# Kernel optimization log

Hardware: AMD Instinct MI355X
Metric: run time of the kernel (lower is better)

The kernel has to match this reference:

```python
import jax, jax.numpy as jnp
import numpy as np


def rotate_half(x):
    d = x.shape[-1] // 2
    return jnp.concatenate([-x[..., d:], x[..., :d]], axis=-1)


def setup_inputs() -> dict:
    key = jax.random.key(0)
    ks = jax.random.split(key, 8)
    B, T, C, H = 2, 2048, 2048, 16
    hd = C // H
    x = jax.random.normal(ks[0], (B, T, C), dtype=jnp.float32)
    # realistic RoPE tables
    inv_freq = 1.0 / (10000.0 ** (jnp.arange(0, hd, 2, dtype=jnp.float32) / hd))
    t = jnp.arange(T, dtype=jnp.float32)
    freqs = jnp.einsum('t,f->tf', t, inv_freq)
    emb = jnp.concatenate([freqs, freqs], axis=-1)  # [T, hd]
    cos = jnp.cos(emb)
    sin = jnp.sin(emb)
    mask = jnp.tril(jnp.ones((T, T), dtype=bool))[None, None]  # causal [1,1,T,T]
    s = C ** -0.5
    Wq = jax.random.normal(ks[1], (C, C), dtype=jnp.float32) * s
    Wk = jax.random.normal(ks[2], (C, C), dtype=jnp.float32) * s
    Wv = jax.random.normal(ks[3], (C, C), dtype=jnp.float32) * s
    Wo = jax.random.normal(ks[4], (C, C), dtype=jnp.float32) * s
    return {"x": x, "cos": cos, "sin": sin, "mask": mask,
            "Wq": Wq, "Wk": Wk, "Wv": Wv, "Wo": Wo}


def reference(x, cos, sin, mask, Wq, Wk, Wv, Wo):
    B, T, C = x.shape
    H = 16
    hd = C // H
    scale = hd ** -0.5
    # projections: torch Linear stores W as [out,in], y = x @ W^T
    def proj(W):
        return jnp.einsum('btc,dc->btd', x, W).reshape(B, T, H, hd).transpose(0, 2, 1, 3)
    q, k, v = proj(Wq), proj(Wk), proj(Wv)  # [B,H,T,hd]
    c = cos[None, None]  # [1,1,T,hd]
    s = sin[None, None]
    q = q * c + rotate_half(q) * s
    k = k * c + rotate_half(k) * s
    attn = jnp.einsum('bhqd,bhkd->bhqk', q, k) * scale
    attn = jnp.where(mask, attn, -jnp.inf)
    attn = jax.nn.softmax(attn, axis=-1)
    out = jnp.einsum('bhqk,bhkd->bhqd', attn, v)
    out = out.transpose(0, 2, 1, 3).reshape(B, T, C)
    return jnp.einsum('btc,dc->btd', out, Wo)
```

## Files before the change

kernel.cpp:

```cpp
#include <hip/hip_runtime.h>
#include <cstdint>

typedef __bf16 bf16_t;
typedef __bf16 bf16x8 __attribute__((ext_vector_type(8)));
typedef __bf16 bf16x4 __attribute__((ext_vector_type(4)));
typedef float  f32x4  __attribute__((ext_vector_type(4)));

#define BB 2
#define TT 2048
#define CC 2048
#define HH 16
#define HD 128

static __device__ __forceinline__ void async_copy16(const void* gp, void* lp) {
  __builtin_amdgcn_global_load_lds(
      (const __attribute__((address_space(1))) void*)(uintptr_t)gp,
      (__attribute__((address_space(3))) void*)(uint32_t)(uintptr_t)lp,
      16, 0, 0);
}

__global__ __launch_bounds__(256)
void cast_all(const float* __restrict__ x, const float* __restrict__ wq,
              const float* __restrict__ wk, const float* __restrict__ wv,
              const float* __restrict__ wo, bf16_t* __restrict__ xb,
              bf16_t* __restrict__ wq_b) {
  const int NX4 = (BB * TT * CC) / 4;
  const int NW4 = (CC * CC) / 4;
  int i = blockIdx.x * 256 + threadIdx.x;
  const float* s;
  bf16_t* d;
  int off;
  if (i < NX4) {
    s = x; d = xb; off = i;
  } else {
    int j = i - NX4;
    int w = j >> 20;
    off = j & (NW4 - 1);
    s = (w == 0) ? wq : (w == 1) ? wk : (w == 2) ? wv : wo;
    d = wq_b + (size_t)w * (CC * CC);
  }
  float4 v = ((const float4*)s)[off];
  bf16x4 o;
  o[0] = (bf16_t)v.x; o[1] = (bf16_t)v.y; o[2] = (bf16_t)v.z; o[3] = (bf16_t)v.w;
  ((bf16x4*)d)[off] = o;
}

__global__ __launch_bounds__(256)
void gemm_v(const bf16_t* __restrict__ A, const bf16_t* __restrict__ Bw,
            bf16_t* __restrict__ C2, int Kdim) {
  __shared__ __align__(16) char smem[128 * 136 * 2];
  bf16_t* As = (bf16_t*)smem;
  bf16_t* Bs = (bf16_t*)(smem + 16384);
  const int tid  = threadIdx.x;
  const int wave = tid >> 6, lane = tid & 63;
  const int quad = lane >> 4, l16 = lane & 15;
  const int m0 = blockIdx.y * 128, n0 = blockIdx.x * 128;
  const int wm = (wave >> 1) * 64, wn = (wave & 1) * 64;

  f32x4 acc[4][4] = {};

  const int srow = lane >> 3;
  const int scol = (((lane & 7) ^ srow) & 7) * 8;
  const int swz  = (l16 & 7) * 8;

  for (int k0 = 0; k0 < Kdim; k0 += 64) {
#pragma unroll
    for (int i = 0; i < 4; ++i) {
      int chunk = wave * 4 + i;
      int row = chunk * 8 + srow;
      async_copy16(A + (size_t)(m0 + row) * Kdim + k0 + scol, As + chunk * 512);
    }
#pragma unroll
    for (int i = 0; i < 4; ++i) {
      int chunk = wave * 4 + i;
      int row = chunk * 8 + srow;
      async_copy16(Bw + (size_t)(n0 + row) * Kdim + k0 + scol, Bs + chunk * 512);
    }
    __syncthreads();
#pragma unroll
    for (int kk = 0; kk < 64; kk += 32) {
      const int koff = (kk + quad * 8) ^ swz;
      bf16x8 af[4], bfr[4];
#pragma unroll
      for (int i = 0; i < 4; ++i)
        af[i] = *(const bf16x8*)&As[(wm + i * 16 + l16) * 64 + koff];
#pragma unroll
      for (int j = 0; j < 4; ++j)
        bfr[j] = *(const bf16x8*)&Bs[(wn + j * 16 + l16) * 64 + koff];
#pragma unroll
      for (int i = 0; i < 4; ++i)
#pragma unroll
        for (int j = 0; j < 4; ++j)
          acc[i][j] = __builtin_amdgcn_mfma_f32_16x16x32_bf16(af[i], bfr[j], acc[i][j], 0, 0, 0);
    }
    __syncthreads();
  }

  const int h = (n0 & (CC - 1)) >> 7;
  bf16_t* Ct = (bf16_t*)smem;
  __syncthreads();
#pragma unroll
  for (int i = 0; i < 4; ++i)
#pragma unroll
    for (int j = 0; j < 4; ++j) {
      int c = wn + j * 16 + l16;
#pragma unroll
      for (int r = 0; r < 4; ++r)
        Ct[(wm + i * 16 + quad * 4 + r) * 136 + c] = (bf16_t)acc[i][j][r];
    }
  __syncthreads();
  const unsigned short* Cu = (const unsigned short*)Ct;
  int col = tid >> 1;
  int rh  = (tid & 1) * 64;
  int grow0 = m0 + rh;
  int b = grow0 >> 11, t0 = grow0 & (TT - 1);
  unsigned int pk[32];
#pragma unroll
  for (int s = 0; s < 32; ++s) {
    unsigned int lo = Cu[(rh + 2 * s) * 136 + col];
    unsigned int hi = Cu[(rh + 2 * s + 1) * 136 + col];
    pk[s] = lo | (hi << 16);
  }
  bf16_t* dstp = C2 + ((size_t)(b * HH + h) * HD + col) * TT + t0;
#pragma unroll
  for (int u = 0; u < 8; ++u) {
    uint4 w; w.x = pk[4*u]; w.y = pk[4*u+1]; w.z = pk[4*u+2]; w.w = pk[4*u+3];
    *(uint4*)(dstp + 8 * u) = w;
  }
}

__global__ __launch_bounds__(512, 2)
void gemm_qkv256(const bf16_t* __restrict__ A, const bf16_t* __restrict__ Bw,
                 bf16_t* __restrict__ Qo, bf16_t* __restrict__ Ko,
                 const float* __restrict__ cosT, const float* __restrict__ sinT,
                 int Kdim) {
  extern __shared__ __align__(16) char smem[];
  bf16_t* lds = (bf16_t*)smem;
  const int tid  = threadIdx.x;
  const int wave = tid >> 6, lane = tid & 63;
  const int quad = lane >> 4, l16 = lane & 15;
  const int wm = wave >> 2, wn = wave & 3;
  const int n0 = blockIdx.x * 256, m0 = blockIdx.y * 256;

  const int srow = lane >> 3;
  const int scol = ((lane & 7) ^ srow) * 8;
  const int swz  = (l16 & 7) * 8;
  const int nK = Kdim >> 6;

  const bf16_t* Ag = A  + (size_t)(m0 + wave * 32 + srow) * Kdim + scol;
  const bf16_t* Bg = Bw + (size_t)(n0 + wave * 32 + srow) * Kdim + scol;
  const int ldsChunk = wave * 4 * 512;

#define STAGE_A(kt, buf)                                                      \
  {                                                                           \
    bf16_t* dstA = lds + (buf) * 32768 + ldsChunk;                            \
    const bf16_t* srcA = Ag + (kt) * 64;                                      \
    _Pragma("unroll")                                                         \
    for (int ci = 0; ci < 4; ++ci)                                            \
      async_copy16(srcA + (size_t)(ci * 8) * Kdim, dstA + ci * 512);          \
  }
#define STAGE_B(kt, buf)                                                      \
  {                                                                           \
    bf16_t* dstB = lds + (buf) * 32768 + 16384 + ldsChunk;                    \
    const bf16_t* srcB = Bg + (kt) * 64;                                      \
    _Pragma("unroll")                                                         \
    for (int ci = 0; ci < 4; ++ci)                                            \
      async_copy16(srcB + (size_t)(ci * 8) * Kdim, dstB + ci * 512);          \
  }

  f32x4 acc[8][4] = {};
  STAGE_A(0, 0); STAGE_B(0, 0); STAGE_A(1, 1); STAGE_B(1, 1);

  const int k0off = (quad * 8) ^ swz;
  const int k1off = (32 + quad * 8) ^ swz;

  for (int k = 0; k < nK; ++k) {
    const int cur = k & 1;
    const bf16_t* Asb = lds + cur * 32768;
    const bf16_t* Bsb = Asb + 16384;
    if (k < nK - 1) asm volatile("s_waitcnt vmcnt(8)" ::: "memory");
    else            asm volatile("s_waitcnt vmcnt(0)" ::: "memory");
    __builtin_amdgcn_s_barrier();
    __builtin_amdgcn_sched_barrier(0);

    bf16x8 a0[8], b0[4], a1[8], b1[4];
#pragma unroll
    for (int i = 0; i < 8; ++i)
      a0[i] = *(const bf16x8*)&Asb[(wm * 128 + i * 16 + l16) * 64 + k0off];
#pragma unroll
    for (int j = 0; j < 4; ++j)
      b0[j] = *(const bf16x8*)&Bsb[(wn * 64 + j * 16 + l16) * 64 + k0off];
    asm volatile("s_waitcnt lgkmcnt(0)" ::: "memory");
    __builtin_amdgcn_sched_barrier(0);
    __builtin_amdgcn_s_setprio(1);
#pragma unroll
    for (int i = 0; i < 4; ++i)
#pragma unroll
      for (int j = 0; j < 4; ++j)
        acc[i][j] = __builtin_amdgcn_mfma_f32_16x16x32_bf16(a0[i], b0[j], acc[i][j], 0, 0, 0);
    __builtin_amdgcn_s_setprio(0);

#pragma unroll
    for (int i = 0; i < 8; ++i)
      a1[i] = *(const bf16x8*)&Asb[(wm * 128 + i * 16 + l16) * 64 + k1off];
#pragma unroll
    for (int j = 0; j < 4; ++j)
      b1[j] = *(const bf16x8*)&Bsb[(wn * 64 + j * 16 + l16) * 64 + k1off];
    __builtin_amdgcn_s_setprio(1);
#pragma unroll
    for (int i = 4; i < 8; ++i)
#pragma unroll
      for (int j = 0; j < 4; ++j)
        acc[i][j] = __builtin_amdgcn_mfma_f32_16x16x32_bf16(a0[i], b0[j], acc[i][j], 0, 0, 0);
    __builtin_amdgcn_s_setprio(0);
    asm volatile("s_waitcnt lgkmcnt(0)" ::: "memory");
    __builtin_amdgcn_s_barrier();
    __builtin_amdgcn_sched_barrier(0);

    if (k + 2 < nK) STAGE_A(k + 2, cur);
    __builtin_amdgcn_s_setprio(1);
#pragma unroll
    for (int i = 0; i < 4; ++i)
#pragma unroll
      for (int j = 0; j < 4; ++j)
        acc[i][j] = __builtin_amdgcn_mfma_f32_16x16x32_bf16(a1[i], b1[j], acc[i][j], 0, 0, 0);
    __builtin_amdgcn_s_setprio(0);

    if (k + 2 < nK) STAGE_B(k + 2, cur);
    __builtin_amdgcn_s_setprio(1);
#pragma unroll
    for (int i = 4; i < 8; ++i)
#pragma unroll
      for (int j = 0; j < 4; ++j)
        acc[i][j] = __builtin_amdgcn_mfma_f32_16x16x32_bf16(a1[i], b1[j], acc[i][j], 0, 0, 0);
    __builtin_amdgcn_s_setprio(0);
  }
#undef STAGE_A
#undef STAGE_B

  {
    const int proj = n0 >> 11;
    bf16_t* dst = proj == 0 ? Qo : Ko;
    bf16_t* Ct = lds;
#pragma unroll
    for (int i = 0; i < 8; ++i)
#pragma unroll
      for (int j = 0; j < 4; ++j) {
        int coll = wn * 64 + j * 16 + l16;
        int pcol = coll + ((coll >> 7) << 2);
#pragma unroll
        for (int r = 0; r < 4; ++r) {
          int rowl = wm * 128 + i * 16 + quad * 4 + r;
          Ct[rowl * 268 + pcol] = (bf16_t)acc[i][j][r];
        }
      }
    __syncthreads();
    const int lane16 = tid & 15;
    const int slot0  = tid >> 4;
    const int d0 = lane16 * 8;
    const int dp = d0 ^ 64;
    const float sgn = (d0 < 64) ? -1.f : 1.f;
    const int b = m0 >> 11;
    const int hbase = (n0 & (CC - 1)) >> 7;
#pragma unroll
    for (int p = 0; p < 16; ++p) {
      int gslot = p * 32 + slot0;
      int rowl = gslot >> 1, hh = gslot & 1;
      int t = (m0 + rowl) & (TT - 1);
      const bf16_t* src = Ct + rowl * 268 + hh * 132;
      bf16x8 self = *(const bf16x8*)(src + d0);
      bf16x8 part = *(const bf16x8*)(src + dp);
      const float* ct = cosT + t * HD + d0;
      const float* st = sinT + t * HD + d0;
      float4 c0 = *(const float4*)(ct);
      float4 c1 = *(const float4*)(ct + 4);
      float4 s0 = *(const float4*)(st);
      float4 s1 = *(const float4*)(st + 4);
      float cc[8] = {c0.x, c0.y, c0.z, c0.w, c1.x, c1.y, c1.z, c1.w};
      float ss[8] = {s0.x, s0.y, s0.z, s0.w, s1.x, s1.y, s1.z, s1.w};
      bf16x8 o8;
#pragma unroll
      for (int e = 0; e < 8; ++e)
        o8[e] = (bf16_t)((float)self[e] * cc[e] + sgn * (float)part[e] * ss[e]);
      *(bf16x8*)(dst + (((size_t)(b * HH + hbase + hh) * TT + t) * HD) + d0) = o8;
    }
  }
}

__global__ __launch_bounds__(512, 2)
void gemm_wo(const bf16_t* __restrict__ A, const bf16_t* __restrict__ Bw,
             float* __restrict__ C, int Kdim) {
  extern __shared__ __align__(16) char smem[];
  bf16_t* lds = (bf16_t*)smem;
  const int tid  = threadIdx.x;
  const int wave = tid >> 6, lane = tid & 63;
  const int quad = lane >> 4, l16 = lane & 15;
  const int wm = wave >> 2, wn = wave & 3;
  const int n0 = blockIdx.x * 256, m0 = blockIdx.y * 128;

  const int srow = lane >> 3;
  const int scol = ((lane & 7) ^ srow) * 8;
  const int swz  = (l16 & 7) * 8;
  const int nK = Kdim >> 6;

#define WSTAGE_A(kt, buf)                                                     \
  {                                                                           \
    bf16_t* d_ = lds + (buf) * 24576;                                         \
    _Pragma("unroll")                                                         \
    for (int c_ = 0; c_ < 2; ++c_) {                                          \
      int ch_ = wave * 2 + c_;                                                \
      async_copy16(A + (size_t)(m0 + ch_ * 8 + srow) * Kdim + (kt) * 64 + scol,\
                   d_ + ch_ * 512);                                           \
    }                                                                         \
  }
#define WSTAGE_B(kt, buf)                                                     \
  {                                                                           \
    bf16_t* d_ = lds + (buf) * 24576 + 8192;                                  \
    _Pragma("unroll")                                                         \
    for (int c_ = 0; c_ < 4; ++c_) {                                          \
      int ch_ = wave * 4 + c_;                                                \
      async_copy16(Bw + (size_t)(n0 + ch_ * 8 + srow) * Kdim + (kt) * 64 + scol,\
                   d_ + ch_ * 512);                                           \
    }                                                                         \
  }

  f32x4 acc[4][4] = {};
  WSTAGE_A(0, 0); WSTAGE_B(0, 0); WSTAGE_A(1, 1); WSTAGE_B(1, 1);

  const int k0off = (quad * 8) ^ swz;
  const int k1off = (32 + quad * 8) ^ swz;

  for (int k = 0; k < nK; ++k) {
    const int cur = k & 1;
    const bf16_t* As = lds + cur * 24576;
    const bf16_t* Bs = As + 8192;
    if (k < nK - 1) asm volatile("s_waitcnt vmcnt(6)" ::: "memory");
    else            asm volatile("s_waitcnt vmcnt(0)" ::: "memory");
    __builtin_amdgcn_s_barrier();
    __builtin_amdgcn_sched_barrier(0);

    bf16x8 a0[4], b0[4], a1[4], b1[4];
#pragma unroll
    for (int i = 0; i < 4; ++i)
      a0[i] = *(const bf16x8*)&As[(wm * 64 + i * 16 + l16) * 64 + k0off];
#pragma unroll
    for (int j = 0; j < 4; ++j)
      b0[j] = *(const bf16x8*)&Bs[(wn * 64 + j * 16 + l16) * 64 + k0off];
    asm volatile("s_waitcnt lgkmcnt(0)" ::: "memory");
    __builtin_amdgcn_sched_barrier(0);
    __builtin_amdgcn_s_setprio(1);
#pragma unroll
    for (int i = 0; i < 4; ++i)
#pragma unroll
      for (int j = 0; j < 2; ++j)
        acc[i][j] = __builtin_amdgcn_mfma_f32_16x16x32_bf16(a0[i], b0[j], acc[i][j], 0, 0, 0);
    __builtin_amdgcn_s_setprio(0);

#pragma unroll
    for (int i = 0; i < 4; ++i)
      a1[i] = *(const bf16x8*)&As[(wm * 64 + i * 16 + l16) * 64 + k1off];
#pragma unroll
    for (int j = 0; j < 4; ++j)
      b1[j] = *(const bf16x8*)&Bs[(wn * 64 + j * 16 + l16) * 64 + k1off];
    __builtin_amdgcn_s_setprio(1);
#pragma unroll
    for (int i = 0; i < 4; ++i)
#pragma unroll
      for (int j = 2; j < 4; ++j)
        acc[i][j] = __builtin_amdgcn_mfma_f32_16x16x32_bf16(a0[i], b0[j], acc[i][j], 0, 0, 0);
    __builtin_amdgcn_s_setprio(0);
    asm volatile("s_waitcnt lgkmcnt(0)" ::: "memory");
    __builtin_amdgcn_s_barrier();
    __builtin_amdgcn_sched_barrier(0);

    if (k + 2 < nK) WSTAGE_A(k + 2, cur);
    __builtin_amdgcn_s_setprio(1);
#pragma unroll
    for (int i = 0; i < 4; ++i)
#pragma unroll
      for (int j = 0; j < 2; ++j)
        acc[i][j] = __builtin_amdgcn_mfma_f32_16x16x32_bf16(a1[i], b1[j], acc[i][j], 0, 0, 0);
    __builtin_amdgcn_s_setprio(0);

    if (k + 2 < nK) WSTAGE_B(k + 2, cur);
    __builtin_amdgcn_s_setprio(1);
#pragma unroll
    for (int i = 0; i < 4; ++i)
#pragma unroll
      for (int j = 2; j < 4; ++j)
        acc[i][j] = __builtin_amdgcn_mfma_f32_16x16x32_bf16(a1[i], b1[j], acc[i][j], 0, 0, 0);
    __builtin_amdgcn_s_setprio(0);
  }
#undef WSTAGE_A
#undef WSTAGE_B

#pragma unroll
  for (int i = 0; i < 4; ++i)
#pragma unroll
    for (int j = 0; j < 4; ++j) {
      int gcol = n0 + wn * 64 + j * 16 + l16;
#pragma unroll
      for (int r = 0; r < 4; ++r) {
        int grow = m0 + wm * 64 + i * 16 + quad * 4 + r;
        C[(size_t)grow * CC + gcol] = acc[i][j][r];
      }
    }
}

__global__ __launch_bounds__(512, 2)
void attn_kernel(const bf16_t* __restrict__ Q, const bf16_t* __restrict__ K,
                 const bf16_t* __restrict__ Vt, bf16_t* __restrict__ Out) {
  __shared__ __align__(16) bf16_t Ks[2][64 * 128];
  __shared__ __align__(16) bf16_t Vs[2][128 * 64];
  __shared__ __align__(16) bf16_t Pl[8][16 * 64];
  const int lane = threadIdx.x & 63, wave = threadIdx.x >> 6;
  const int quad = lane >> 4, l16 = lane & 15;
  const int linear = blockIdx.x;
  const int hb = linear & 31;
  const int h = hb & (HH - 1), b = hb >> 4;
  const int spair = linear >> 5;
  const size_t qkbase = (size_t)(b * HH + h) * TT * HD;
  const bf16_t* Kh = K + qkbase;
  const bf16_t* Vh = Vt + (size_t)(b * HH + h) * HD * TT;
  const float scale = 0.08838834764831845f;

  const int srK = lane >> 4;
  const int sgK = lane & 15;
  const int scK0 = (sgK ^ srK) * 8;
  const int scK1 = (sgK ^ (4 + srK)) * 8;
  const int srV = lane >> 3;
  const int scV = (((lane & 7) ^ srV) & 7) * 8;
  const int swz = (l16 & 7) * 8;
  const int psw = (l16 & 7) << 3;

#pragma unroll
  for (int half = 0; half < 2; ++half) {
    const int qt = half == 0 ? (15 - spair) : spair;
    const int q0 = qt * 128 + wave * 16;
    const int nIter = qt * 2 + 2;

    bf16x8 qf[4];
    {
      const bf16_t* qrow = Q + qkbase + (size_t)(q0 + l16) * HD;
#pragma unroll
      for (int kc = 0; kc < 4; ++kc) qf[kc] = *(const bf16x8*)(qrow + kc * 32 + quad * 8);
    }

    f32x4 o[8] = {};
    float l_i[4] = {};

    {
#pragma unroll
      for (int i = 0; i < 2; ++i) {
        int chunk = wave * 2 + i;
        int sc = (chunk & 1) ? scK1 : scK0;
        async_copy16(Kh + (size_t)(chunk * 4 + srK) * HD + sc, &Ks[0][chunk * 512]);
      }
#pragma unroll
      for (int i = 0; i < 2; ++i) {
        int chunk = wave * 2 + i;
        async_copy16(Vh + (size_t)(chunk * 8 + srV) * TT + scV, &Vs[0][chunk * 512]);
      }
    }

    for (int it = 0; it < nIter; ++it) {
      const int cur = it & 1;
      const int key0 = it * 64;
      __syncthreads();

      if (it + 1 < nIter) {
        const int nxt = cur ^ 1;
        const int knxt = key0 + 64;
#pragma unroll
        for (int i = 0; i < 2; ++i) {
          int chunk = wave * 2 + i;
          int sc = (chunk & 1) ? scK1 : scK0;
          async_copy16(Kh + (size_t)(knxt + chunk * 4 + srK) * HD + sc, &Ks[nxt][chunk * 512]);
        }
#pragma unroll
        for (int i = 0; i < 2; ++i) {
          int chunk = wave * 2 + i;
          async_copy16(Vh + (size_t)(chunk * 8 + srV) * TT + knxt + scV, &Vs[nxt][chunk * 512]);
        }
      }

      f32x4 s[4] = {};
#pragma unroll
      for (int kc = 0; kc < 4; ++kc) {
        const int koff = (kc * 32 + quad * 8) ^ swz;
#pragma unroll
        for (int kt = 0; kt < 4; ++kt) {
          bf16x8 kf = *(const bf16x8*)&Ks[cur][(kt * 16 + l16) * 128 + koff];
          s[kt] = __builtin_amdgcn_mfma_f32_16x16x32_bf16(qf[kc], kf, s[kt], 0, 0, 0);
        }
      }

      {
        bf16_t* pl = &Pl[wave][0];
#pragma unroll
        for (int r = 0; r < 4; ++r) {
          int prow = quad * 4 + r;
          int rel = q0 + prow - key0;
          int rbase = prow * 64;
          int sw = (prow & 7) << 3;
          float lr = 0.f;
#pragma unroll
          for (int kt = 0; kt < 4; ++kt) {
            int c16 = kt * 16 + l16;
            float e = (c16 > rel) ? 0.f : __expf(s[kt][r] * scale);
            lr += e;
            pl[rbase + (c16 ^ sw)] = (bf16_t)e;
          }
          l_i[r] += lr;
        }
      }

      bf16x8 pf0 = *(const bf16x8*)&Pl[wave][l16 * 64 + ((quad * 8) ^ psw)];
      bf16x8 pf1 = *(const bf16x8*)&Pl[wave][l16 * 64 + ((32 + quad * 8) ^ psw)];
      const int voff0 = (quad * 8) ^ swz;
      const int voff1 = (32 + quad * 8) ^ swz;
#pragma unroll
      for (int n = 0; n < 8; ++n) {
        bf16x8 vf0 = *(const bf16x8*)&Vs[cur][(n * 16 + l16) * 64 + voff0];
        bf16x8 vf1 = *(const bf16x8*)&Vs[cur][(n * 16 + l16) * 64 + voff1];
        o[n] = __builtin_amdgcn_mfma_f32_16x16x32_bf16(pf0, vf0, o[n], 0, 0, 0);
        o[n] = __builtin_amdgcn_mfma_f32_16x16x32_bf16(pf1, vf1, o[n], 0, 0, 0);
      }
    }

#pragma unroll
    for (int r = 0; r < 4; ++r) {
      float l = l_i[r];
#pragma unroll
      for (int off = 1; off < 16; off <<= 1) l += __shfl_xor(l, off);
      l_i[r] = 1.f / l;
    }

#pragma unroll
    for (int n = 0; n < 8; ++n)
#pragma unroll
      for (int r = 0; r < 4; ++r) {
        int qg = q0 + quad * 4 + r;
        size_t off = ((size_t)(b * TT + qg) * CC) + h * HD + n * 16 + l16;
        Out[off] = (bf16_t)(o[n][r] * l_i[r]);
      }
  }
}

extern "C" void kernel_launch(void* const* d_in, const int* in_sizes, int n_in,
                              void* d_out, int out_size, void* d_ws, size_t ws_size,
                              hipStream_t stream) {
  const float* x    = (const float*)d_in[0];
  const float* cosT = (const float*)d_in[1];
  const float* sinT = (const float*)d_in[2];
  const float* Wq = (const float*)d_in[4];
  const float* Wk = (const float*)d_in[5];
  const float* Wv = (const float*)d_in[6];
  const float* Wo = (const float*)d_in[7];
  float* out = (float*)d_out;

  char* ws = (char*)d_ws;
  const size_t XSZ = (size_t)BB * TT * CC * 2;
  const size_t WSZ = (size_t)CC * CC * 2;
  bf16_t* x_bf  = (bf16_t*)(ws);
  bf16_t* wq_bf = (bf16_t*)(ws + XSZ);
  bf16_t* wv_bf = (bf16_t*)(ws + XSZ + 2 * WSZ);
  bf16_t* wo_bf = (bf16_t*)(ws + XSZ + 3 * WSZ);
  bf16_t* Qb    = (bf16_t*)(ws + XSZ + 4 * WSZ);
  bf16_t* Kb    = (bf16_t*)(ws + 2 * XSZ + 4 * WSZ);
  bf16_t* Vt    = (bf16_t*)(ws + 3 * XSZ + 4 * WSZ);
  bf16_t* attn_bf = x_bf;

  const int NX = BB * TT * CC;
  const int NW = CC * CC;
  cast_all<<<(NX / 4 + 4 * (NW / 4)) / 256, 256, 0, stream>>>(
      x, Wq, Wk, Wv, Wo, x_bf, wq_bf);

  (void)hipFuncSetAttribute(reinterpret_cast<const void*>(gemm_qkv256),
                            hipFuncAttributeMaxDynamicSharedMemorySize, 137216);
  gemm_qkv256<<<dim3(2 * CC / 256, BB * TT / 256), 512, 137216, stream>>>(
      x_bf, wq_bf, Qb, Kb, cosT, sinT, CC);

  gemm_v<<<dim3(CC / 128, BB * TT / 128), 256, 0, stream>>>(
      x_bf, wv_bf, Vt, CC);

  attn_kernel<<<dim3(BB * HH * 8), 512, 0, stream>>>(Qb, Kb, Vt, attn_bf);

  (void)hipFuncSetAttribute(reinterpret_cast<const void*>(gemm_wo),
                            hipFuncAttributeMaxDynamicSharedMemorySize, 98304);
  gemm_wo<<<dim3(CC / 256, BB * TT / 128), 512, 98304, stream>>>(
      attn_bf, wo_bf, out, CC);
}
```

Baseline: 351.9 us.

## Replace V projection GEMM with double-buffered 128x256 pipelined kernel

Replaces the simple single-buffered 128x128 gemm_v, which waits on a barrier after each K step, with a 512-thread 128x256-tile kernel modelled on gemm_wo. The new kernel double-buffers LDS loads, interleaves async global-to-LDS prefetch with MFMA phases, and uses s_setprio to favour the matrix instructions. It keeps the transposed Vt output through an LDS staging pass. The aim is to hide global load latency and raise MFMA utilisation for the V projection, at the cost of more LDS per block and hand-tuned waitcnt logic.

```diff
diff --git a/kernel.cpp b/kernel.cpp
--- a/kernel.cpp
+++ b/kernel.cpp
@@ -45,90 +45,6 @@
   ((bf16x4*)d)[off] = o;
 }
 
-__global__ __launch_bounds__(256)
-void gemm_v(const bf16_t* __restrict__ A, const bf16_t* __restrict__ Bw,
-            bf16_t* __restrict__ C2, int Kdim) {
-  __shared__ __align__(16) char smem[128 * 136 * 2];
-  bf16_t* As = (bf16_t*)smem;
-  bf16_t* Bs = (bf16_t*)(smem + 16384);
-  const int tid  = threadIdx.x;
-  const int wave = tid >> 6, lane = tid & 63;
-  const int quad = lane >> 4, l16 = lane & 15;
-  const int m0 = blockIdx.y * 128, n0 = blockIdx.x * 128;
-  const int wm = (wave >> 1) * 64, wn = (wave & 1) * 64;
-
-  f32x4 acc[4][4] = {};
-
-  const int srow = lane >> 3;
-  const int scol = (((lane & 7) ^ srow) & 7) * 8;
-  const int swz  = (l16 & 7) * 8;
-
-  for (int k0 = 0; k0 < Kdim; k0 += 64) {
-#pragma unroll
-    for (int i = 0; i < 4; ++i) {
-      int chunk = wave * 4 + i;
-      int row = chunk * 8 + srow;
-      async_copy16(A + (size_t)(m0 + row) * Kdim + k0 + scol, As + chunk * 512);
-    }
-#pragma unroll
-    for (int i = 0; i < 4; ++i) {
-      int chunk = wave * 4 + i;
-      int row = chunk * 8 + srow;
-      async_copy16(Bw + (size_t)(n0 + row) * Kdim + k0 + scol, Bs + chunk * 512);
-    }
-    __syncthreads();
-#pragma unroll
-    for (int kk = 0; kk < 64; kk += 32) {
-      const int koff = (kk + quad * 8) ^ swz;
-      bf16x8 af[4], bfr[4];
-#pragma unroll
-      for (int i = 0; i < 4; ++i)
-        af[i] = *(const bf16x8*)&As[(wm + i * 16 + l16) * 64 + koff];
-#pragma unroll
-      for (int j = 0; j < 4; ++j)
-        bfr[j] = *(const bf16x8*)&Bs[(wn + j * 16 + l16) * 64 + koff];
-#pragma unroll
-      for (int i = 0; i < 4; ++i)
-#pragma unroll
-        for (int j = 0; j < 4; ++j)
-          acc[i][j] = __builtin_amdgcn_mfma_f32_16x16x32_bf16(af[i], bfr[j], acc[i][j], 0, 0, 0);
-    }
-    __syncthreads();
-  }
-
-  const int h = (n0 & (CC - 1)) >> 7;
-  bf16_t* Ct = (bf16_t*)smem;
-  __syncthreads();
-#pragma unroll
-  for (int i = 0; i < 4; ++i)
-#pragma unroll
-    for (int j = 0; j < 4; ++j) {
-      int c = wn + j * 16 + l16;
-#pragma unroll
-      for (int r = 0; r < 4; ++r)
-        Ct[(wm + i * 16 + quad * 4 + r) * 136 + c] = (bf16_t)acc[i][j][r];
-    }
-  __syncthreads();
-  const unsigned short* Cu = (const unsigned short*)Ct;
-  int col = tid >> 1;
-  int rh  = (tid & 1) * 64;
-  int grow0 = m0 + rh;
-  int b = grow0 >> 11, t0 = grow0 & (TT - 1);
-  unsigned int pk[32];
-#pragma unroll
-  for (int s = 0; s < 32; ++s) {
-    unsigned int lo = Cu[(rh + 2 * s) * 136 + col];
-    unsigned int hi = Cu[(rh + 2 * s + 1) * 136 + col];
-    pk[s] = lo | (hi << 16);
-  }
-  bf16_t* dstp = C2 + ((size_t)(b * HH + h) * HD + col) * TT + t0;
-#pragma unroll
-  for (int u = 0; u < 8; ++u) {
-    uint4 w; w.x = pk[4*u]; w.y = pk[4*u+1]; w.z = pk[4*u+2]; w.w = pk[4*u+3];
-    *(uint4*)(dstp + 8 * u) = w;
-  }
-}
-
 __global__ __launch_bounds__(512, 2)
 void gemm_qkv256(const bf16_t* __restrict__ A, const bf16_t* __restrict__ Bw,
                  bf16_t* __restrict__ Qo, bf16_t* __restrict__ Ko,
@@ -288,6 +204,149 @@
 }
 
 __global__ __launch_bounds__(512, 2)
+void gemm_v256(const bf16_t* __restrict__ A, const bf16_t* __restrict__ Bw,
+               bf16_t* __restrict__ Vt, int Kdim) {
+  extern __shared__ __align__(16) char smem[];
+  bf16_t* lds = (bf16_t*)smem;
+  const int tid  = threadIdx.x;
+  const int wave = tid >> 6, lane = tid & 63;
+  const int quad = lane >> 4, l16 = lane & 15;
+  const int wm = wave >> 2, wn = wave & 3;
+  const int n0 = blockIdx.x * 256, m0 = blockIdx.y * 128;
+
+  const int srow = lane >> 3;
+  const int scol = ((lane & 7) ^ srow) * 8;
+  const int swz  = (l16 & 7) * 8;
+  const int nK = Kdim >> 6;
+
+#define VSTAGE_A(kt, buf)                                                     \
+  {                                                                           \
+    bf16_t* d_ = lds + (buf) * 24576;                                         \
+    _Pragma("unroll")                                                         \
+    for (int c_ = 0; c_ < 2; ++c_) {                                          \
+      int ch_ = wave * 2 + c_;                                                \
+      async_copy16(A + (size_t)(m0 + ch_ * 8 + srow) * Kdim + (kt) * 64 + scol,\
+                   d_ + ch_ * 512);                                           \
+    }                                                                         \
+  }
+#define VSTAGE_B(kt, buf)                                                     \
+  {                                                                           \
+    bf16_t* d_ = lds + (buf) * 24576 + 8192;                                  \
+    _Pragma("unroll")                                                         \
+    for (int c_ = 0; c_ < 4; ++c_) {                                          \
+      int ch_ = wave * 4 + c_;                                                \
+      async_copy16(Bw + (size_t)(n0 + ch_ * 8 + srow) * Kdim + (kt) * 64 + scol,\
+                   d_ + ch_ * 512);                                           \
+    }                                                                         \
+  }
+
+  f32x4 acc[4][4] = {};
+  VSTAGE_A(0, 0); VSTAGE_B(0, 0); VSTAGE_A(1, 1); VSTAGE_B(1, 1);
+
+  const int k0off = (quad * 8) ^ swz;
+  const int k1off = (32 + quad * 8) ^ swz;
+
+  for (int k = 0; k < nK; ++k) {
+    const int cur = k & 1;
+    const bf16_t* As = lds + cur * 24576;
+    const bf16_t* Bs = As + 8192;
+    if (k < nK - 1) asm volatile("s_waitcnt vmcnt(6)" ::: "memory");
+    else            asm volatile("s_waitcnt vmcnt(0)" ::: "memory");
+    __builtin_amdgcn_s_barrier();
+    __builtin_amdgcn_sched_barrier(0);
+
+    bf16x8 a0[4], b0[4], a1[4], b1[4];
+#pragma unroll
+    for (int i = 0; i < 4; ++i)
+      a0[i] = *(const bf16x8*)&As[(wm * 64 + i * 16 + l16) * 64 + k0off];
+#pragma unroll
+    for (int j = 0; j < 4; ++j)
+      b0[j] = *(const bf16x8*)&Bs[(wn * 64 + j * 16 + l16) * 64 + k0off];
+    asm volatile("s_waitcnt lgkmcnt(0)" ::: "memory");
+    __builtin_amdgcn_sched_barrier(0);
+    __builtin_amdgcn_s_setprio(1);
+#pragma unroll
+    for (int i = 0; i < 4; ++i)
+#pragma unroll
+      for (int j = 0; j < 2; ++j)
+        acc[i][j] = __builtin_amdgcn_mfma_f32_16x16x32_bf16(a0[i], b0[j], acc[i][j], 0, 0, 0);
+    __builtin_amdgcn_s_setprio(0);
+
+#pragma unroll
+    for (int i = 0; i < 4; ++i)
+      a1[i] = *(const bf16x8*)&As[(wm * 64 + i * 16 + l16) * 64 + k1off];
+#pragma unroll
+    for (int j = 0; j < 4; ++j)
+      b1[j] = *(const bf16x8*)&Bs[(wn * 64 + j * 16 + l16) * 64 + k1off];
+    __builtin_amdgcn_s_setprio(1);
+#pragma unroll
+    for (int i = 0; i < 4; ++i)
+#pragma unroll
+      for (int j = 2; j < 4; ++j)
+        acc[i][j] = __builtin_amdgcn_mfma_f32_16x16x32_bf16(a0[i], b0[j], acc[i][j], 0, 0, 0);
+    __builtin_amdgcn_s_setprio(0);
+    asm volatile("s_waitcnt lgkmcnt(0)" ::: "memory");
+    __builtin_amdgcn_s_barrier();
+    __builtin_amdgcn_sched_barrier(0);
+
+    if (k + 2 < nK) VSTAGE_A(k + 2, cur);
+    __builtin_amdgcn_s_setprio(1);
+#pragma unroll
+    for (int i = 0; i < 4; ++i)
+#pragma unroll
+      for (int j = 0; j < 2; ++j)
+        acc[i][j] = __builtin_amdgcn_mfma_f32_16x16x32_bf16(a1[i], b1[j], acc[i][j], 0, 0, 0);
+    __builtin_amdgcn_s_setprio(0);
+
+    if (k + 2 < nK) VSTAGE_B(k + 2, cur);
+    __builtin_amdgcn_s_setprio(1);
+#pragma unroll
+    for (int i = 0; i < 4; ++i)
+#pragma unroll
+      for (int j = 2; j < 4; ++j)
+        acc[i][j] = __builtin_amdgcn_mfma_f32_16x16x32_bf16(a1[i], b1[j], acc[i][j], 0, 0, 0);
+    __builtin_amdgcn_s_setprio(0);
+  }
+#undef VSTAGE_A
+#undef VSTAGE_B
+
+  __syncthreads();
+  {
+    bf16_t* Ct = lds;
+#pragma unroll
+    for (int i = 0; i < 4; ++i)
+#pragma unroll
+      for (int j = 0; j < 4; ++j) {
+        int c = wn * 64 + j * 16 + l16;
+#pragma unroll
+        for (int r = 0; r < 4; ++r)
+          Ct[(wm * 64 + i * 16 + quad * 4 + r) * 264 + c] = (bf16_t)acc[i][j][r];
+      }
+    __syncthreads();
+    const unsigned short* Cu = (const unsigned short*)Ct;
+    int col = tid >> 1;
+    int rh  = (tid & 1) * 64;
+    int dv = n0 + col;
+    int h = dv >> 7, d = dv & (HD - 1);
+    int b = m0 >> 11;
+    int t0 = (m0 & (TT - 1)) + rh;
+    unsigned int pk[32];
+#pragma unroll
+    for (int s = 0; s < 32; ++s) {
+      unsigned int lo = Cu[(rh + 2 * s) * 264 + col];
+      unsigned int hi = Cu[(rh + 2 * s + 1) * 264 + col];
+      pk[s] = lo | (hi << 16);
+    }
+    bf16_t* dstp = Vt + ((size_t)(b * HH + h) * HD + d) * TT + t0;
+#pragma unroll
+    for (int u = 0; u < 8; ++u) {
+      uint4 w; w.x = pk[4*u]; w.y = pk[4*u+1]; w.z = pk[4*u+2]; w.w = pk[4*u+3];
+      *(uint4*)(dstp + 8 * u) = w;
+    }
+  }
+}
+
+__global__ __launch_bounds__(512, 2)
 void gemm_wo(const bf16_t* __restrict__ A, const bf16_t* __restrict__ Bw,
              float* __restrict__ C, int Kdim) {
   extern __shared__ __align__(16) char smem[];
@@ -581,7 +640,9 @@
   gemm_qkv256<<<dim3(2 * CC / 256, BB * TT / 256), 512, 137216, stream>>>(
       x_bf, wq_bf, Qb, Kb, cosT, sinT, CC);
 
-  gemm_v<<<dim3(CC / 128, BB * TT / 128), 256, 0, stream>>>(
+  (void)hipFuncSetAttribute(reinterpret_cast<const void*>(gemm_v256),
+                            hipFuncAttributeMaxDynamicSharedMemorySize, 98304);
+  gemm_v256<<<dim3(CC / 256, BB * TT / 128), 512, 98304, stream>>>(
       x_bf, wv_bf, Vt, CC);
 
   attn_kernel<<<dim3(BB * HH * 8), 512, 0, stream>>>(Qb, Kb, Vt, attn_bf);
```

Measured after the change: 352.8 us. Within noise of the previous version (+0.3%).
